# Performance work log

Measured on AMD Instinct MI355X. Metric: run time of the kernel, lower is better.

## Reference

```python
import jax, jax.numpy as jnp
import numpy as np

B, T, D = 1, 2048, 2048
H, HD = 16, 128          # n_heads, head_dim
RD = 64                  # rotary_emb_dim
K = 4                    # short conv kernel size
EPS = 1e-5


def setup_inputs() -> dict:
    key = jax.random.key(0)
    ks = jax.random.split(key, 10)
    hidden_states = jax.random.normal(ks[0], (B, T, D), dtype=jnp.float32)
    # standard RoPE tables for the rotary sub-dimension
    inv_freq = 1.0 / (10000.0 ** (jnp.arange(0, RD, 2, dtype=jnp.float32) / RD))  # [RD/2]
    pos = jnp.arange(T, dtype=jnp.float32)
    freqs = pos[:, None] * inv_freq[None, :]          # [T, RD/2]
    emb = jnp.concatenate([freqs, freqs], axis=-1)    # [T, RD]
    cos = jnp.broadcast_to(jnp.cos(emb)[None], (B, T, RD))
    sin = jnp.broadcast_to(jnp.sin(emb)[None], (B, T, RD))
    s = 1.0 / np.sqrt(D)
    return {
        "hidden_states": hidden_states,
        "cos": cos, "sin": sin,
        "Wq": jax.random.normal(ks[1], (D, D), jnp.float32) * s,
        "Wk": jax.random.normal(ks[2], (D, D), jnp.float32) * s,
        "Wv": jax.random.normal(ks[3], (D, D), jnp.float32) * s,
        "Wo": jax.random.normal(ks[4], (D, D), jnp.float32) * s,
        "conv_q_w": jax.random.normal(ks[5], (D, K), jnp.float32) * 0.5,
        "conv_k_w": jax.random.normal(ks[6], (D, K), jnp.float32) * 0.5,
        "conv_v_w": jax.random.normal(ks[7], (D, K), jnp.float32) * 0.5,
        "q_norm_w": jnp.ones((HD,), jnp.float32),
        "k_norm_w": jnp.ones((HD,), jnp.float32),
    }


def _causal_conv_silu(x, w):
    # x: [B,T,D], w: [D,K]; depthwise causal conv (tap K-1 hits current pos) + SiLU
    xp = jnp.pad(x, ((0, 0), (K - 1, 0), (0, 0)))
    y = sum(xp[:, j:j + T, :] * w[None, None, :, j] for j in range(K))
    return jax.nn.silu(y)


def _rms_norm(x, w):
    # x: [..., HD]
    var = jnp.mean(x * x, axis=-1, keepdims=True)
    return x * jax.lax.rsqrt(var + EPS) * w


def _rotate_half(x):
    x1, x2 = x[..., : x.shape[-1] // 2], x[..., x.shape[-1] // 2:]
    return jnp.concatenate([-x2, x1], axis=-1)


def _apply_rope(x, cos, sin):
    # x: [B,H,T,HD]; cos/sin: [B,T,RD] -> unsqueeze head dim; partial rotary branch
    cos = cos[:, None, :, :]
    sin = sin[:, None, :, :]
    x_rot, x_pass = x[..., :RD], x[..., RD:]
    x_rot = x_rot * cos + _rotate_half(x_rot) * sin
    # faithful to source: negates rotated part when rotary_dim != head_dim
    return jnp.concatenate([-x_rot, x_pass], axis=-1)


def reference(hidden_states, cos, sin, Wq, Wk, Wv, Wo,
              conv_q_w, conv_k_w, conv_v_w, q_norm_w, k_norm_w):
    # projections (Linear with bias=False: y = x @ W^T)
    q = hidden_states @ Wq.T
    k = hidden_states @ Wk.T
    v = hidden_states @ Wv.T
    # short causal depthwise conv + SiLU
    q = _causal_conv_silu(q, conv_q_w)
    k = _causal_conv_silu(k, conv_k_w)
    v = _causal_conv_silu(v, conv_v_w)
    # split heads: [B,T,D] -> [B,T,H,HD]
    q = q.reshape(B, T, H, HD)
    k = k.reshape(B, T, H, HD)
    v = v.reshape(B, T, H, HD)
    # per-head RMSNorm, then [B,H,T,HD]
    q = _rms_norm(q, q_norm_w).transpose(0, 2, 1, 3)
    k = _rms_norm(k, k_norm_w).transpose(0, 2, 1, 3)
    v = v.transpose(0, 2, 1, 3)
    # RoPE (partial)
    q = _apply_rope(q, cos, sin)
    k = _apply_rope(k, cos, sin)
    # causal attention
    scale = 1.0 / np.sqrt(HD)
    scores = jnp.einsum('bhqd,bhkd->bhqk', q, k) * scale
    causal = jnp.tril(jnp.ones((T, T), dtype=bool))
    scores = jnp.where(causal[None, None], scores, jnp.float32(-1e30))
    probs = jax.nn.softmax(scores, axis=-1)
    attn = jnp.einsum('bhqk,bhkd->bhqd', probs, v)
    # [B,H,T,HD] -> [B,T,D], output projection
    out = attn.transpose(0, 2, 1, 3).reshape(B, T, D) @ Wo.T
    return out
```

## Files before the change

### kernel.cpp

```cpp
#include <hip/hip_runtime.h>
#include <hip/hip_bf16.h>

#define T_SEQ 2048
#define D_MODEL 2048
#define NH 16
#define HDIM 128
#define RD_ROT 64

typedef __bf16 bf16x8 __attribute__((ext_vector_type(8)));
typedef float f32x4 __attribute__((ext_vector_type(4)));

__device__ __forceinline__ void async_copy16(const __bf16* g, __bf16* l) {
    __builtin_amdgcn_global_load_lds(
        (const __attribute__((address_space(1))) void*)g,
        (__attribute__((address_space(3))) void*)l, 16, 0, 0);
}

__global__ __launch_bounds__(256) void cast_kernel(
    const float* __restrict__ s0, const float* __restrict__ s1, const float* __restrict__ s2,
    const float* __restrict__ s3, const float* __restrict__ s4,
    __bf16* __restrict__ d0, __bf16* __restrict__ d1, __bf16* __restrict__ d2,
    __bf16* __restrict__ d3, __bf16* __restrict__ d4)
{
    const float* s; __bf16* d;
    switch (blockIdx.y) {
        case 0: s = s0; d = d0; break;
        case 1: s = s1; d = d1; break;
        case 2: s = s2; d = d2; break;
        case 3: s = s3; d = d3; break;
        default: s = s4; d = d4; break;
    }
    size_t base = (size_t)blockIdx.x * D_MODEL + (size_t)threadIdx.x * 8;
    f32x4 a = *(const f32x4*)(s + base);
    f32x4 b = *(const f32x4*)(s + base + 4);
    bf16x8 o;
    #pragma unroll
    for (int i = 0; i < 4; i++) { o[i] = (__bf16)a[i]; o[i + 4] = (__bf16)b[i]; }
    *(bf16x8*)(d + base) = o;
}

__device__ __forceinline__ bf16x8 ld_frag(const __bf16* lds, int rr, int s, int quad, int r7) {
    return *(const bf16x8*)&lds[rr * 64 + ((((s << 2) + quad) ^ r7) << 3)];
}

__global__ __launch_bounds__(512, 2) void gemm_qkv_pipe_kernel(
    const __bf16* __restrict__ A,
    const __bf16* __restrict__ B0, const __bf16* __restrict__ B1, const __bf16* __restrict__ B2,
    __bf16* __restrict__ C0, __bf16* __restrict__ C1, __bf16* __restrict__ C2)
{
    constexpr int BM = 256, BK = 64, KD = D_MODEL, NT = KD / BK;

    __shared__ __align__(16) __bf16 As[2][BM * BK];
    __shared__ __align__(16) __bf16 Bs[2][BM * BK];

    const int flat = (int)blockIdx.x + 8 * ((int)blockIdx.y + 8 * (int)blockIdx.z);
    const int swz  = (flat & 7) * 24 + (flat >> 3);
    const int bz   = swz >> 6;
    const int bm   = (swz & 7) * BM;
    const int bn   = ((swz >> 3) & 7) * BM;

    const __bf16* Bmat = bz == 0 ? B0 : (bz == 1 ? B1 : B2);
    __bf16* Cmat       = bz == 0 ? C0 : (bz == 1 ? C1 : C2);

    const int tid  = threadIdx.x;
    const int lane = tid & 63;
    const int wave = tid >> 6;
    const int r15  = lane & 15;
    const int quad = lane >> 4;
    const int r7   = r15 & 7;
    const int wm   = wave >> 2;
    const int wn   = wave & 3;

    const int sr8 = lane >> 3;
    const int sck = (lane & 7) ^ sr8;
    const __bf16* Ap = A    + (size_t)(bm + wave * 16 + sr8) * KD + sck * 8;
    const __bf16* Bp = Bmat + (size_t)(bn + wave * 16 + sr8) * KD + sck * 8;

    auto stageA = [&](int buf, int h, int kt) {
        const __bf16* s = Ap + (size_t)(h * 128) * KD + kt;
        __bf16* d = &As[buf][h * 8192 + wave * 1024];
        async_copy16(s, d);
        async_copy16(s + 8 * KD, d + 512);
    };
    auto stageB = [&](int buf, int h, int kt) {
        const __bf16* s = Bp + (size_t)(h * 128) * KD + kt;
        __bf16* d = &Bs[buf][h * 8192 + wave * 1024];
        async_copy16(s, d);
        async_copy16(s + 8 * KD, d + 512);
    };

    f32x4 acc[8][4] = {};
    bf16x8 a0[4][2], a1[4][2], b0[2][2], b1[2][2];

    auto mfma16 = [&](int mb, int nb, bf16x8 (&av)[4][2], bf16x8 (&bv)[2][2]) {
        #pragma unroll
        for (int mf = 0; mf < 4; mf++)
            #pragma unroll
            for (int nf = 0; nf < 2; nf++)
                #pragma unroll
                for (int s = 0; s < 2; s++)
                    acc[mb + mf][nb + nf] =
                        __builtin_amdgcn_mfma_f32_16x16x32_bf16(av[mf][s], bv[nf][s], acc[mb + mf][nb + nf], 0, 0, 0);
    };

    stageB(0, 0, 0);  stageB(0, 1, 0);  stageA(0, 0, 0);  stageA(0, 1, 0);
    stageB(1, 0, BK); stageB(1, 1, BK); stageA(1, 0, BK); stageA(1, 1, BK);
    asm volatile("s_waitcnt vmcnt(8)" ::: "memory");
    __builtin_amdgcn_s_barrier();
    __builtin_amdgcn_sched_barrier(0);
    #pragma unroll
    for (int mf = 0; mf < 4; mf++)
        #pragma unroll
        for (int s = 0; s < 2; s++)
            a0[mf][s] = ld_frag(As[0], wm * 128 + mf * 16 + r15, s, quad, r7);
    #pragma unroll
    for (int nf = 0; nf < 2; nf++)
        #pragma unroll
        for (int s = 0; s < 2; s++)
            b0[nf][s] = ld_frag(Bs[0], wn * 64 + nf * 16 + r15, s, quad, r7);

    for (int t = 0; t < NT; t++) {
        const int b = t & 1;
        const __bf16* Asb = As[b];
        const __bf16* Bsb = Bs[b];
        const __bf16* Aso = As[b ^ 1];
        const __bf16* Bso = Bs[b ^ 1];
        const bool pf = (t + 2 < NT);
        const int ktp = (t + 2) * BK;

        #pragma unroll
        for (int nf = 0; nf < 2; nf++)
            #pragma unroll
            for (int s = 0; s < 2; s++)
                b1[nf][s] = ld_frag(Bsb, wn * 64 + 32 + nf * 16 + r15, s, quad, r7);
        __builtin_amdgcn_sched_barrier(0);
        __builtin_amdgcn_s_setprio(1);
        mfma16(0, 0, a0, b0);
        __builtin_amdgcn_s_setprio(0);
        __builtin_amdgcn_sched_barrier(0);
        __builtin_amdgcn_s_barrier();
        __builtin_amdgcn_sched_barrier(0);

        #pragma unroll
        for (int mf = 0; mf < 4; mf++)
            #pragma unroll
            for (int s = 0; s < 2; s++)
                a1[mf][s] = ld_frag(Asb, wm * 128 + 64 + mf * 16 + r15, s, quad, r7);
        __builtin_amdgcn_sched_barrier(0);
        __builtin_amdgcn_s_setprio(1);
        mfma16(0, 2, a0, b1);
        __builtin_amdgcn_s_setprio(0);
        __builtin_amdgcn_sched_barrier(0);
        __builtin_amdgcn_s_barrier();
        __builtin_amdgcn_sched_barrier(0);

        if (pf) { stageB(b, 0, ktp); stageB(b, 1, ktp); }
        __builtin_amdgcn_sched_barrier(0);
        __builtin_amdgcn_s_setprio(1);
        mfma16(4, 2, a1, b1);
        __builtin_amdgcn_s_setprio(0);
        __builtin_amdgcn_sched_barrier(0);
        if (pf) asm volatile("s_waitcnt vmcnt(4)" ::: "memory");
        else    asm volatile("s_waitcnt vmcnt(0)" ::: "memory");
        __builtin_amdgcn_s_barrier();
        __builtin_amdgcn_sched_barrier(0);

        #pragma unroll
        for (int mf = 0; mf < 4; mf++)
            #pragma unroll
            for (int s = 0; s < 2; s++)
                a0[mf][s] = ld_frag(Aso, wm * 128 + mf * 16 + r15, s, quad, r7);
        if (pf) { stageA(b, 0, ktp); stageA(b, 1, ktp); }
        __builtin_amdgcn_sched_barrier(0);
        __builtin_amdgcn_s_setprio(1);
        mfma16(4, 0, a1, b0);
        __builtin_amdgcn_s_setprio(0);
        __builtin_amdgcn_sched_barrier(0);
        #pragma unroll
        for (int nf = 0; nf < 2; nf++)
            #pragma unroll
            for (int s = 0; s < 2; s++)
                b0[nf][s] = ld_frag(Bso, wn * 64 + nf * 16 + r15, s, quad, r7);
        __builtin_amdgcn_sched_barrier(0);
        __builtin_amdgcn_s_barrier();
        __builtin_amdgcn_sched_barrier(0);
    }

    #pragma unroll
    for (int mf = 0; mf < 8; mf++) {
        #pragma unroll
        for (int r = 0; r < 4; r++) {
            const size_t row = (size_t)(bm + wm * 128 + mf * 16 + quad * 4 + r);
            #pragma unroll
            for (int nf = 0; nf < 4; nf++) {
                const size_t col = (size_t)(bn + wn * 64 + nf * 16 + r15);
                Cmat[row * D_MODEL + col] = (__bf16)acc[mf][nf][r];
            }
        }
    }
}

__global__ __launch_bounds__(256) void proj_gemm_kernel(
    const __bf16* __restrict__ A, const __bf16* __restrict__ Bmat, float* __restrict__ C)
{
    constexpr int BM = 128, BK = 64, KD = D_MODEL, NT = KD / BK;

    __shared__ __align__(16) __bf16 As[2][BM * BK];
    __shared__ __align__(16) __bf16 Bs[2][BM * BK];

    const int flat = (int)blockIdx.x + 16 * (int)blockIdx.y;
    const int swz  = (flat & 7) * 32 + (flat >> 3);
    const int bm   = (swz & 15) * BM;
    const int bn   = (swz >> 4) * BM;

    const int tid  = threadIdx.x;
    const int lane = tid & 63;
    const int wave = tid >> 6;
    const int r15  = lane & 15;
    const int quad = lane >> 4;
    const int r7   = r15 & 7;
    const int wm   = (wave >> 1) * 64;
    const int wn   = (wave & 1) * 64;

    const int sr8 = lane >> 3;
    const int sck = (lane & 7) ^ sr8;
    const __bf16* Ap = A    + (size_t)(bm + wave * 8 + sr8) * KD + sck * 8;
    const __bf16* Bp = Bmat + (size_t)(bn + wave * 8 + sr8) * KD + sck * 8;

    auto stageA = [&](int buf, int kt) {
        #pragma unroll
        for (int j = 0; j < 4; j++)
            async_copy16(Ap + (size_t)(j * 32) * KD + kt, &As[buf][wave * 512 + j * 2048]);
    };
    auto stageB = [&](int buf, int kt) {
        #pragma unroll
        for (int j = 0; j < 4; j++)
            async_copy16(Bp + (size_t)(j * 32) * KD + kt, &Bs[buf][wave * 512 + j * 2048]);
    };

    f32x4 acc[4][4] = {};
    bf16x8 a0[2][2], a1[2][2], b0[2][2], b1[2][2];

    auto mfma8 = [&](int mb, int nb, bf16x8 (&av)[2][2], bf16x8 (&bv)[2][2]) {
        #pragma unroll
        for (int mf = 0; mf < 2; mf++)
            #pragma unroll
            for (int nf = 0; nf < 2; nf++)
                #pragma unroll
                for (int s = 0; s < 2; s++)
                    acc[mb + mf][nb + nf] =
                        __builtin_amdgcn_mfma_f32_16x16x32_bf16(av[mf][s], bv[nf][s], acc[mb + mf][nb + nf], 0, 0, 0);
    };

    stageB(0, 0);  stageA(0, 0);
    stageB(1, BK); stageA(1, BK);
    asm volatile("s_waitcnt vmcnt(8)" ::: "memory");
    __builtin_amdgcn_s_barrier();
    __builtin_amdgcn_sched_barrier(0);
    #pragma unroll
    for (int mf = 0; mf < 2; mf++)
        #pragma unroll
        for (int s = 0; s < 2; s++)
            a0[mf][s] = ld_frag(As[0], wm + mf * 16 + r15, s, quad, r7);
    #pragma unroll
    for (int nf = 0; nf < 2; nf++)
        #pragma unroll
        for (int s = 0; s < 2; s++)
            b0[nf][s] = ld_frag(Bs[0], wn + nf * 16 + r15, s, quad, r7);

    for (int t = 0; t < NT; t++) {
        const int b = t & 1;
        const __bf16* Asb = As[b];
        const __bf16* Bsb = Bs[b];
        const __bf16* Aso = As[b ^ 1];
        const __bf16* Bso = Bs[b ^ 1];
        const bool pf = (t + 2 < NT);
        const bool rd = (t + 1 < NT);
        const int ktp = (t + 2) * BK;

        #pragma unroll
        for (int nf = 0; nf < 2; nf++)
            #pragma unroll
            for (int s = 0; s < 2; s++)
                b1[nf][s] = ld_frag(Bsb, wn + 32 + nf * 16 + r15, s, quad, r7);
        __builtin_amdgcn_sched_barrier(0);
        __builtin_amdgcn_s_setprio(1);
        mfma8(0, 0, a0, b0);
        __builtin_amdgcn_s_setprio(0);
        __builtin_amdgcn_sched_barrier(0);
        __builtin_amdgcn_s_barrier();
        __builtin_amdgcn_sched_barrier(0);

        if (pf) stageB(b, ktp);
        #pragma unroll
        for (int mf = 0; mf < 2; mf++)
            #pragma unroll
            for (int s = 0; s < 2; s++)
                a1[mf][s] = ld_frag(Asb, wm + 32 + mf * 16 + r15, s, quad, r7);
        __builtin_amdgcn_sched_barrier(0);
        __builtin_amdgcn_s_setprio(1);
        mfma8(0, 2, a0, b1);
        __builtin_amdgcn_s_setprio(0);
        __builtin_amdgcn_sched_barrier(0);
        if (pf) asm volatile("s_waitcnt vmcnt(4)" ::: "memory");
        else    asm volatile("s_waitcnt vmcnt(0)" ::: "memory");
        __builtin_amdgcn_s_barrier();
        __builtin_amdgcn_sched_barrier(0);

        if (rd)
            #pragma unroll
            for (int mf = 0; mf < 2; mf++)
                #pragma unroll
                for (int s = 0; s < 2; s++)
                    a0[mf][s] = ld_frag(Aso, wm + mf * 16 + r15, s, quad, r7);
        if (pf) stageA(b, ktp);
        __builtin_amdgcn_sched_barrier(0);
        __builtin_amdgcn_s_setprio(1);
        mfma8(2, 2, a1, b1);
        __builtin_amdgcn_s_setprio(0);
        __builtin_amdgcn_sched_barrier(0);
        __builtin_amdgcn_s_barrier();
        __builtin_amdgcn_sched_barrier(0);

        __builtin_amdgcn_s_setprio(1);
        mfma8(2, 0, a1, b0);
        __builtin_amdgcn_s_setprio(0);
        __builtin_amdgcn_sched_barrier(0);
        if (rd)
            #pragma unroll
            for (int nf = 0; nf < 2; nf++)
                #pragma unroll
                for (int s = 0; s < 2; s++)
                    b0[nf][s] = ld_frag(Bso, wn + nf * 16 + r15, s, quad, r7);
        __builtin_amdgcn_sched_barrier(0);
        __builtin_amdgcn_s_barrier();
        __builtin_amdgcn_sched_barrier(0);
    }

    #pragma unroll
    for (int mf = 0; mf < 4; mf++) {
        #pragma unroll
        for (int r = 0; r < 4; r++) {
            const size_t row = (size_t)(bm + wm + mf * 16 + quad * 4 + r);
            #pragma unroll
            for (int nf = 0; nf < 4; nf++) {
                const size_t col = (size_t)(bn + wn + nf * 16 + r15);
                C[row * D_MODEL + col] = acc[mf][nf][r];
            }
        }
    }
}

__global__ __launch_bounds__(256) void preproc_qk_kernel(
    const __bf16* __restrict__ q_raw, const __bf16* __restrict__ k_raw,
    const float* __restrict__ cwq, const float* __restrict__ cwk,
    const float* __restrict__ qnw, const float* __restrict__ knw,
    const float* __restrict__ cosb, const float* __restrict__ sinb,
    __bf16* __restrict__ q_proc, __bf16* __restrict__ k_proc)
{
    const int t = blockIdx.x;
    const int which = blockIdx.y;
    const __bf16* X = which ? k_raw : q_raw;
    const float*  W = which ? cwk : cwq;
    const float*  nw = which ? knw : qnw;
    __bf16* P = which ? k_proc : q_proc;
    const float SC = which ? 1.0f : 0.08838834764831845f;

    const int tid = threadIdx.x;
    const int c0  = tid * 8;
    const int h   = tid >> 4;
    const int dl0 = (tid & 15) * 8;

    f32x4 wv[8];
    #pragma unroll
    for (int i = 0; i < 8; i++) wv[i] = *(const f32x4*)&W[(c0 + i) * 4];

    float acc[8] = {};
    #pragma unroll
    for (int j = 0; j < 4; j++) {
        int tt = t + j - 3;
        if (tt >= 0) {
            bf16x8 xv = *(const bf16x8*)&X[(size_t)tt * D_MODEL + c0];
            #pragma unroll
            for (int i = 0; i < 8; i++) acc[i] += (float)xv[i] * wv[i][j];
        }
    }
    float sil[8], ss = 0.f;
    #pragma unroll
    for (int i = 0; i < 8; i++) {
        float s = acc[i] / (1.f + __expf(-acc[i]));
        sil[i] = s; ss += s * s;
    }
    #pragma unroll
    for (int off = 1; off < 16; off <<= 1) ss += __shfl_xor(ss, off);
    float inv = rsqrtf(ss * (1.f / 128.f) + 1e-5f);

    f32x4 nv0 = *(const f32x4*)&nw[dl0];
    f32x4 nv1 = *(const f32x4*)&nw[dl0 + 4];
    float yn[8];
    #pragma unroll
    for (int i = 0; i < 8; i++) yn[i] = sil[i] * inv * (i < 4 ? nv0[i] : nv1[i - 4]);

    float partner[8];
    #pragma unroll
    for (int i = 0; i < 8; i++) partner[i] = __shfl_xor(yn[i], 4);

    bf16x8 o;
    if (dl0 < RD_ROT) {
        f32x4 cv0 = *(const f32x4*)&cosb[t * RD_ROT + dl0];
        f32x4 cv1 = *(const f32x4*)&cosb[t * RD_ROT + dl0 + 4];
        f32x4 sv0 = *(const f32x4*)&sinb[t * RD_ROT + dl0];
        f32x4 sv1 = *(const f32x4*)&sinb[t * RD_ROT + dl0 + 4];
        #pragma unroll
        for (int i = 0; i < 8; i++) {
            int dl = dl0 + i;
            float c = i < 4 ? cv0[i] : cv1[i - 4];
            float s = i < 4 ? sv0[i] : sv1[i - 4];
            float rot = (dl < 32) ? -partner[i] : partner[i];
            o[i] = (__bf16)((yn[i] * c + rot * s) * SC);
        }
    } else {
        #pragma unroll
        for (int i = 0; i < 8; i++) o[i] = (__bf16)(yn[i] * SC);
    }
    *(bf16x8*)&P[((size_t)h * T_SEQ + t) * HDIM + dl0] = o;
}

__global__ __launch_bounds__(128) void preproc_v_kernel(
    const __bf16* __restrict__ v_raw, const float* __restrict__ cwv,
    __bf16* __restrict__ v_t)
{
    const int t0 = blockIdx.x * 8;
    const int h = blockIdx.y;
    const int dl = threadIdx.x;
    const int d = h * HDIM + dl;

    f32x4 wv = *(const f32x4*)&cwv[d * 4];
    float x[11];
    #pragma unroll
    for (int m = 0; m < 11; m++) {
        int tt = t0 - 3 + m;
        x[m] = (tt >= 0) ? (float)v_raw[(size_t)tt * D_MODEL + d] : 0.f;
    }
    bf16x8 o;
    #pragma unroll
    for (int r = 0; r < 8; r++) {
        float y = x[r] * wv[0] + x[r + 1] * wv[1] + x[r + 2] * wv[2] + x[r + 3] * wv[3];
        o[r] = (__bf16)(y / (1.f + __expf(-y)));
    }
    *(bf16x8*)&v_t[((size_t)h * HDIM + dl) * T_SEQ + t0] = o;
}

__global__ __launch_bounds__(256, 2) void attn_kernel(
    const __bf16* __restrict__ Qp,
    const __bf16* __restrict__ Kp,
    const __bf16* __restrict__ Vt,
    __bf16* __restrict__ Op)
{
    constexpr int TK = 64, PSTR = 72;
    __shared__ __align__(16) __bf16 Ks[2][TK * HDIM];
    __shared__ __align__(16) __bf16 Vs[2][HDIM * TK];
    __shared__ __align__(16) __bf16 Ps[64 * PSTR];

    const int lane = threadIdx.x & 63;
    const int wave = threadIdx.x >> 6;
    const int r15  = lane & 15;
    const int quad = lane >> 4;
    const int h = blockIdx.y;
    const int qi = (blockIdx.y & 8) ? ((int)gridDim.x - 1 - (int)blockIdx.x) : (int)blockIdx.x;
    const int q0 = qi * TK;

    const __bf16* Kb = Kp + (size_t)h * T_SEQ * HDIM;
    const __bf16* Vb = Vt + (size_t)h * HDIM * T_SEQ;

    const int kchunk = wave * 4;
    const int krow_l = (lane >> 4);
    const int kg     = lane & 15;
    const int vrow_l = (lane >> 3);
    const int vg     = lane & 7;

    auto stage_tile = [&](int tile, int sb) {
        const int tkn = tile * TK;
        #pragma unroll
        for (int i = 0; i < 4; i++) {
            int ck = kchunk + i;
            int krow = ck * 4 + krow_l;
            int vrow = ck * 8 + vrow_l;
            async_copy16(Kb + (size_t)(tkn + krow) * HDIM + (kg ^ (krow & 15)) * 8, &Ks[sb][ck * 512]);
            async_copy16(Vb + (size_t)vrow * T_SEQ + tkn + (vg ^ (vrow & 7)) * 8, &Vs[sb][ck * 512]);
        }
    };

    bf16x8 qf[4];
    const __bf16* qbase = Qp + ((size_t)h * T_SEQ + q0 + wave * 16 + r15) * HDIM;
    #pragma unroll
    for (int s = 0; s < 4; s++) qf[s] = *(const bf16x8*)(qbase + s * 32 + quad * 8);

    f32x4 oacc[8] = {};
    float lsum[4] = {};

    const int ntk = qi + 1;

    stage_tile(0, 0);
    if (ntk > 1) stage_tile(1, 1);

    for (int it = 0; it < ntk; it++) {
        const int buf = it & 1;
        const bool last = (it == ntk - 1);

        if (last) asm volatile("s_waitcnt vmcnt(0)" ::: "memory");
        else      asm volatile("s_waitcnt vmcnt(8)" ::: "memory");
        __builtin_amdgcn_s_barrier();

        f32x4 sacc[4] = {};
        #pragma unroll
        for (int s = 0; s < 4; s++) {
            #pragma unroll
            for (int nt = 0; nt < 4; nt++) {
                bf16x8 kf = *(const bf16x8*)&Ks[buf][(nt * 16 + r15) * HDIM + (((s * 4 + quad) ^ r15) << 3)];
                sacc[nt] = __builtin_amdgcn_mfma_f32_16x16x32_bf16(qf[s], kf, sacc[nt], 0, 0, 0);
            }
        }

        #pragma unroll
        for (int nt = 0; nt < 4; nt++) {
            #pragma unroll
            for (int r = 0; r < 4; r++) {
                float p = __expf(sacc[nt][r]);
                if (last) {
                    int qrow = q0 + wave * 16 + quad * 4 + r;
                    int kcol = it * TK + nt * 16 + r15;
                    if (kcol > qrow) p = 0.f;
                }
                sacc[nt][r] = p;
                lsum[r] += p;
            }
        }

        #pragma unroll
        for (int nt = 0; nt < 4; nt++)
            #pragma unroll
            for (int r = 0; r < 4; r++)
                Ps[(wave * 16 + quad * 4 + r) * PSTR + nt * 16 + r15] = (__bf16)sacc[nt][r];

        #pragma unroll
        for (int s2 = 0; s2 < 2; s2++) {
            bf16x8 pf = *(const bf16x8*)&Ps[(wave * 16 + r15) * PSTR + s2 * 32 + quad * 8];
            #pragma unroll
            for (int nt = 0; nt < 8; nt++) {
                bf16x8 vf = *(const bf16x8*)&Vs[buf][(nt * 16 + r15) * TK + (((s2 * 4 + quad) ^ (r15 & 7)) << 3)];
                oacc[nt] = __builtin_amdgcn_mfma_f32_16x16x32_bf16(pf, vf, oacc[nt], 0, 0, 0);
            }
        }

        __builtin_amdgcn_s_barrier();
        if (it + 2 < ntk) stage_tile(it + 2, buf);
    }

    #pragma unroll
    for (int r = 0; r < 4; r++) {
        float l = lsum[r];
        #pragma unroll
        for (int off = 1; off < 16; off <<= 1) l += __shfl_xor(l, off);
        float inv = 1.0f / l;
        size_t row = q0 + wave * 16 + quad * 4 + r;
        #pragma unroll
        for (int nt = 0; nt < 8; nt++)
            Op[row * D_MODEL + h * HDIM + nt * 16 + r15] = (__bf16)(oacc[nt][r] * inv);
    }
}

extern "C" void kernel_launch(void* const* d_in, const int* in_sizes, int n_in,
                              void* d_out, int out_size, void* d_ws, size_t ws_size,
                              hipStream_t stream) {
    (void)in_sizes; (void)n_in; (void)out_size; (void)ws_size;
    const float* hidden = (const float*)d_in[0];
    const float* cosb   = (const float*)d_in[1];
    const float* sinb   = (const float*)d_in[2];
    const float* Wq     = (const float*)d_in[3];
    const float* Wk     = (const float*)d_in[4];
    const float* Wv     = (const float*)d_in[5];
    const float* Wo     = (const float*)d_in[6];
    const float* cwq    = (const float*)d_in[7];
    const float* cwk    = (const float*)d_in[8];
    const float* cwv    = (const float*)d_in[9];
    const float* qnw    = (const float*)d_in[10];
    const float* knw    = (const float*)d_in[11];

    const size_t NEL = (size_t)T_SEQ * D_MODEL;
    __bf16* ws = (__bf16*)d_ws;
    __bf16* h_bf   = ws + 0 * NEL;
    __bf16* Wq_bf  = ws + 1 * NEL;
    __bf16* Wk_bf  = ws + 2 * NEL;
    __bf16* Wv_bf  = ws + 3 * NEL;
    __bf16* Wo_bf  = ws + 4 * NEL;
    __bf16* q_raw  = ws + 5 * NEL;
    __bf16* k_raw  = ws + 6 * NEL;
    __bf16* v_raw  = ws + 7 * NEL;
    __bf16* q_proc = Wq_bf;
    __bf16* k_proc = Wk_bf;
    __bf16* v_t    = Wv_bf;
    __bf16* attn_b = h_bf;
    float*  out    = (float*)d_out;

    cast_kernel<<<dim3(T_SEQ, 5), 256, 0, stream>>>(hidden, Wq, Wk, Wv, Wo,
                                                    h_bf, Wq_bf, Wk_bf, Wv_bf, Wo_bf);
    gemm_qkv_pipe_kernel<<<dim3(8, 8, 3), 512, 0, stream>>>(
        h_bf, Wq_bf, Wk_bf, Wv_bf, q_raw, k_raw, v_raw);
    preproc_qk_kernel<<<dim3(T_SEQ, 2), 256, 0, stream>>>(
        q_raw, k_raw, cwq, cwk, qnw, knw, cosb, sinb, q_proc, k_proc);
    preproc_v_kernel<<<dim3(T_SEQ / 8, NH), 128, 0, stream>>>(v_raw, cwv, v_t);
    attn_kernel<<<dim3(T_SEQ / 64, NH), 256, 0, stream>>>(q_proc, k_proc, v_t, attn_b);
    proj_gemm_kernel<<<dim3(16, 16), 256, 0, stream>>>(attn_b, Wo_bf, out);
}
```

Baseline: 309.8 us.

## Fuse QKV GEMMs into one 256x192-tile GEMM over concatenated weights

Treats Wq/Wk/Wv as one contiguous 6144-row weight matrix and q/k/v outputs as one contiguous buffer. A single 2D grid of 8x32 blocks uses a 256x192 tile, which gives 256 blocks instead of 192. The main loop is restructured into two alternating tile steps with double-buffered B fragments and fewer barriers per k-step. It relies on the workspace layout putting Wq/Wk/Wv and q/k/v_raw next to each other, and it drops the block-index swizzle, so L2 locality may change.

```diff
diff --git a/kernel.cpp b/kernel.cpp
--- a/kernel.cpp
+++ b/kernel.cpp
@@ -43,24 +43,18 @@
     return *(const bf16x8*)&lds[rr * 64 + ((((s << 2) + quad) ^ r7) << 3)];
 }
 
-__global__ __launch_bounds__(512, 2) void gemm_qkv_pipe_kernel(
+__global__ __launch_bounds__(512, 2) void gemm_qkv_fused_kernel(
     const __bf16* __restrict__ A,
-    const __bf16* __restrict__ B0, const __bf16* __restrict__ B1, const __bf16* __restrict__ B2,
-    __bf16* __restrict__ C0, __bf16* __restrict__ C1, __bf16* __restrict__ C2)
+    const __bf16* __restrict__ Bf,
+    __bf16* __restrict__ Cf)
 {
-    constexpr int BM = 256, BK = 64, KD = D_MODEL, NT = KD / BK;
+    constexpr int BM = 256, BN = 192, BK = 64, KD = D_MODEL, NT = KD / BK;
 
     __shared__ __align__(16) __bf16 As[2][BM * BK];
-    __shared__ __align__(16) __bf16 Bs[2][BM * BK];
-
-    const int flat = (int)blockIdx.x + 8 * ((int)blockIdx.y + 8 * (int)blockIdx.z);
-    const int swz  = (flat & 7) * 24 + (flat >> 3);
-    const int bz   = swz >> 6;
-    const int bm   = (swz & 7) * BM;
-    const int bn   = ((swz >> 3) & 7) * BM;
-
-    const __bf16* Bmat = bz == 0 ? B0 : (bz == 1 ? B1 : B2);
-    __bf16* Cmat       = bz == 0 ? C0 : (bz == 1 ? C1 : C2);
+    __shared__ __align__(16) __bf16 Bs[2][BN * BK];
+
+    const int bm = (int)blockIdx.x * BM;
+    const int bn = (int)blockIdx.y * BN;
 
     const int tid  = threadIdx.x;
     const int lane = tid & 63;
@@ -73,128 +67,116 @@
 
     const int sr8 = lane >> 3;
     const int sck = (lane & 7) ^ sr8;
-    const __bf16* Ap = A    + (size_t)(bm + wave * 16 + sr8) * KD + sck * 8;
-    const __bf16* Bp = Bmat + (size_t)(bn + wave * 16 + sr8) * KD + sck * 8;
-
-    auto stageA = [&](int buf, int h, int kt) {
-        const __bf16* s = Ap + (size_t)(h * 128) * KD + kt;
-        __bf16* d = &As[buf][h * 8192 + wave * 1024];
-        async_copy16(s, d);
-        async_copy16(s + 8 * KD, d + 512);
-    };
-    auto stageB = [&](int buf, int h, int kt) {
-        const __bf16* s = Bp + (size_t)(h * 128) * KD + kt;
-        __bf16* d = &Bs[buf][h * 8192 + wave * 1024];
-        async_copy16(s, d);
-        async_copy16(s + 8 * KD, d + 512);
-    };
-
-    f32x4 acc[8][4] = {};
-    bf16x8 a0[4][2], a1[4][2], b0[2][2], b1[2][2];
-
-    auto mfma16 = [&](int mb, int nb, bf16x8 (&av)[4][2], bf16x8 (&bv)[2][2]) {
-        #pragma unroll
-        for (int mf = 0; mf < 4; mf++)
-            #pragma unroll
-            for (int nf = 0; nf < 2; nf++)
-                #pragma unroll
-                for (int s = 0; s < 2; s++)
-                    acc[mb + mf][nb + nf] =
-                        __builtin_amdgcn_mfma_f32_16x16x32_bf16(av[mf][s], bv[nf][s], acc[mb + mf][nb + nf], 0, 0, 0);
-    };
-
-    stageB(0, 0, 0);  stageB(0, 1, 0);  stageA(0, 0, 0);  stageA(0, 1, 0);
-    stageB(1, 0, BK); stageB(1, 1, BK); stageA(1, 0, BK); stageA(1, 1, BK);
-    asm volatile("s_waitcnt vmcnt(8)" ::: "memory");
-    __builtin_amdgcn_s_barrier();
-    __builtin_amdgcn_sched_barrier(0);
-    #pragma unroll
-    for (int mf = 0; mf < 4; mf++)
-        #pragma unroll
-        for (int s = 0; s < 2; s++)
-            a0[mf][s] = ld_frag(As[0], wm * 128 + mf * 16 + r15, s, quad, r7);
-    #pragma unroll
-    for (int nf = 0; nf < 2; nf++)
-        #pragma unroll
-        for (int s = 0; s < 2; s++)
-            b0[nf][s] = ld_frag(Bs[0], wn * 64 + nf * 16 + r15, s, quad, r7);
-
-    for (int t = 0; t < NT; t++) {
+    const __bf16* Ap = A  + (size_t)(bm + wave * 8 + sr8) * KD + sck * 8;
+    const __bf16* Bp = Bf + (size_t)(bn + wave * 8 + sr8) * KD + sck * 8;
+
+    auto stageA = [&](int buf, int kt) {
+        #pragma unroll
+        for (int j = 0; j < 4; j++)
+            async_copy16(Ap + (size_t)(j * 64) * KD + kt, &As[buf][j * 4096 + wave * 512]);
+    };
+    auto stageB = [&](int buf, int kt) {
+        #pragma unroll
+        for (int j = 0; j < 3; j++)
+            async_copy16(Bp + (size_t)(j * 64) * KD + kt, &Bs[buf][j * 4096 + wave * 512]);
+    };
+
+    f32x4 acc[8][3] = {};
+    bf16x8 a0[4][2], a1[4][2];
+    bf16x8 bE[3][2], bO[3][2];
+
+    auto tile_step = [&](int t, bf16x8 (&bc)[3][2], bf16x8 (&bnx)[3][2]) {
         const int b = t & 1;
         const __bf16* Asb = As[b];
-        const __bf16* Bsb = Bs[b];
         const __bf16* Aso = As[b ^ 1];
         const __bf16* Bso = Bs[b ^ 1];
         const bool pf = (t + 2 < NT);
+        const bool rd = (t + 1 < NT);
         const int ktp = (t + 2) * BK;
-
-        #pragma unroll
-        for (int nf = 0; nf < 2; nf++)
-            #pragma unroll
-            for (int s = 0; s < 2; s++)
-                b1[nf][s] = ld_frag(Bsb, wn * 64 + 32 + nf * 16 + r15, s, quad, r7);
-        __builtin_amdgcn_sched_barrier(0);
-        __builtin_amdgcn_s_setprio(1);
-        mfma16(0, 0, a0, b0);
-        __builtin_amdgcn_s_setprio(0);
-        __builtin_amdgcn_sched_barrier(0);
-        __builtin_amdgcn_s_barrier();
-        __builtin_amdgcn_sched_barrier(0);
 
         #pragma unroll
         for (int mf = 0; mf < 4; mf++)
             #pragma unroll
             for (int s = 0; s < 2; s++)
                 a1[mf][s] = ld_frag(Asb, wm * 128 + 64 + mf * 16 + r15, s, quad, r7);
+        if (pf) stageB(b, ktp);
         __builtin_amdgcn_sched_barrier(0);
         __builtin_amdgcn_s_setprio(1);
-        mfma16(0, 2, a0, b1);
+        #pragma unroll
+        for (int mf = 0; mf < 4; mf++)
+            #pragma unroll
+            for (int nf = 0; nf < 3; nf++)
+                #pragma unroll
+                for (int s = 0; s < 2; s++)
+                    acc[mf][nf] = __builtin_amdgcn_mfma_f32_16x16x32_bf16(a0[mf][s], bc[nf][s], acc[mf][nf], 0, 0, 0);
         __builtin_amdgcn_s_setprio(0);
         __builtin_amdgcn_sched_barrier(0);
-        __builtin_amdgcn_s_barrier();
-        __builtin_amdgcn_sched_barrier(0);
-
-        if (pf) { stageB(b, 0, ktp); stageB(b, 1, ktp); }
+        if (pf) asm volatile("s_waitcnt vmcnt(3)" ::: "memory");
+        else    asm volatile("s_waitcnt vmcnt(0)" ::: "memory");
+        __builtin_amdgcn_s_barrier();
+        __builtin_amdgcn_sched_barrier(0);
+
+        if (rd) {
+            #pragma unroll
+            for (int nf = 0; nf < 3; nf++)
+                #pragma unroll
+                for (int s = 0; s < 2; s++)
+                    bnx[nf][s] = ld_frag(Bso, wn * 48 + nf * 16 + r15, s, quad, r7);
+            #pragma unroll
+            for (int mf = 0; mf < 4; mf++)
+                #pragma unroll
+                for (int s = 0; s < 2; s++)
+                    a0[mf][s] = ld_frag(Aso, wm * 128 + mf * 16 + r15, s, quad, r7);
+        }
+        if (pf) stageA(b, ktp);
         __builtin_amdgcn_sched_barrier(0);
         __builtin_amdgcn_s_setprio(1);
-        mfma16(4, 2, a1, b1);
+        #pragma unroll
+        for (int mf = 0; mf < 4; mf++)
+            #pragma unroll
+            for (int nf = 0; nf < 3; nf++)
+                #pragma unroll
+                for (int s = 0; s < 2; s++)
+                    acc[4 + mf][nf] = __builtin_amdgcn_mfma_f32_16x16x32_bf16(a1[mf][s], bc[nf][s], acc[4 + mf][nf], 0, 0, 0);
         __builtin_amdgcn_s_setprio(0);
         __builtin_amdgcn_sched_barrier(0);
-        if (pf) asm volatile("s_waitcnt vmcnt(4)" ::: "memory");
-        else    asm volatile("s_waitcnt vmcnt(0)" ::: "memory");
-        __builtin_amdgcn_s_barrier();
-        __builtin_amdgcn_sched_barrier(0);
-
-        #pragma unroll
-        for (int mf = 0; mf < 4; mf++)
-            #pragma unroll
-            for (int s = 0; s < 2; s++)
-                a0[mf][s] = ld_frag(Aso, wm * 128 + mf * 16 + r15, s, quad, r7);
-        if (pf) { stageA(b, 0, ktp); stageA(b, 1, ktp); }
-        __builtin_amdgcn_sched_barrier(0);
-        __builtin_amdgcn_s_setprio(1);
-        mfma16(4, 0, a1, b0);
-        __builtin_amdgcn_s_setprio(0);
-        __builtin_amdgcn_sched_barrier(0);
-        #pragma unroll
-        for (int nf = 0; nf < 2; nf++)
-            #pragma unroll
-            for (int s = 0; s < 2; s++)
-                b0[nf][s] = ld_frag(Bso, wn * 64 + nf * 16 + r15, s, quad, r7);
-        __builtin_amdgcn_sched_barrier(0);
-        __builtin_amdgcn_s_barrier();
-        __builtin_amdgcn_sched_barrier(0);
-    }
-
-    #pragma unroll
-    for (int mf = 0; mf < 8; mf++) {
-        #pragma unroll
-        for (int r = 0; r < 4; r++) {
-            const size_t row = (size_t)(bm + wm * 128 + mf * 16 + quad * 4 + r);
-            #pragma unroll
-            for (int nf = 0; nf < 4; nf++) {
-                const size_t col = (size_t)(bn + wn * 64 + nf * 16 + r15);
-                Cmat[row * D_MODEL + col] = (__bf16)acc[mf][nf][r];
+        __builtin_amdgcn_s_barrier();
+        __builtin_amdgcn_sched_barrier(0);
+    };
+
+    stageB(0, 0);  stageA(0, 0);
+    stageB(1, BK); stageA(1, BK);
+    asm volatile("s_waitcnt vmcnt(7)" ::: "memory");
+    __builtin_amdgcn_s_barrier();
+    __builtin_amdgcn_sched_barrier(0);
+    #pragma unroll
+    for (int nf = 0; nf < 3; nf++)
+        #pragma unroll
+        for (int s = 0; s < 2; s++)
+            bE[nf][s] = ld_frag(Bs[0], wn * 48 + nf * 16 + r15, s, quad, r7);
+    #pragma unroll
+    for (int mf = 0; mf < 4; mf++)
+        #pragma unroll
+        for (int s = 0; s < 2; s++)
+            a0[mf][s] = ld_frag(As[0], wm * 128 + mf * 16 + r15, s, quad, r7);
+
+    for (int t = 0; t < NT; t += 2) {
+        tile_step(t,     bE, bO);
+        tile_step(t + 1, bO, bE);
+    }
+
+    #pragma unroll
+    for (int nf = 0; nf < 3; nf++) {
+        const int col0 = bn + wn * 48 + nf * 16;
+        const int mat  = col0 >> 11;
+        const int colr = (col0 & 2047) + r15;
+        __bf16* Cm = Cf + (size_t)mat * T_SEQ * D_MODEL;
+        #pragma unroll
+        for (int mf = 0; mf < 8; mf++) {
+            #pragma unroll
+            for (int r = 0; r < 4; r++) {
+                const size_t row = (size_t)(bm + wm * 128 + mf * 16 + quad * 4 + r);
+                Cm[row * D_MODEL + colr] = (__bf16)acc[mf][nf][r];
             }
         }
     }
@@ -605,8 +587,7 @@
 
     cast_kernel<<<dim3(T_SEQ, 5), 256, 0, stream>>>(hidden, Wq, Wk, Wv, Wo,
                                                     h_bf, Wq_bf, Wk_bf, Wv_bf, Wo_bf);
-    gemm_qkv_pipe_kernel<<<dim3(8, 8, 3), 512, 0, stream>>>(
-        h_bf, Wq_bf, Wk_bf, Wv_bf, q_raw, k_raw, v_raw);
+    gemm_qkv_fused_kernel<<<dim3(8, 32), 512, 0, stream>>>(h_bf, Wq_bf, q_raw);
     preproc_qk_kernel<<<dim3(T_SEQ, 2), 256, 0, stream>>>(
         q_raw, k_raw, cwq, cwk, qnw, knw, cosb, sinb, q_proc, k_proc);
     preproc_v_kernel<<<dim3(T_SEQ / 8, NH), 128, 0, stream>>>(v_raw, cwv, v_t);
```

Result: no change. 305.2 us (-1.5%).
